# Kernel tuning notes

Hardware: AMD Instinct MI355X
Metric: run time of the kernel (lower is better)

The kernel has to match this reference:

```python
import jax, jax.numpy as jnp
import numpy as np
from jax import lax

N_LAYERS = 30
KERNEL = 5
MU = 255.0  # quantization_channels=256 -> mu = 255
DILATIONS = [(2 ** k) % 10 for k in range(N_LAYERS)]  # 2^k mod (n_layers/n_cycles)


def causal_conv1d(x, w, b, dilation):
    # x: [B,1,T], w: [1,1,K], b: [1]; left-pad so output is causal, same length.
    pad = (w.shape[-1] - 1) * dilation
    xp = jnp.pad(x, ((0, 0), (0, 0), (pad, 0)))
    y = lax.conv_general_dilated(xp, w, window_strides=(1,), padding='VALID',
                                 rhs_dilation=(dilation,),
                                 dimension_numbers=('NCH', 'OIH', 'NCH'))
    return y + b[None, :, None]


def setup_inputs() -> dict:
    key = jax.random.key(0)
    ks = jax.random.split(key, 12)
    B, T = 8, 262144
    s = 0.2  # keep gated activations away from saturation
    return {
        'x': jax.random.normal(ks[0], (B, 1, T), dtype=jnp.float32),
        'causal_w': jax.random.normal(ks[1], (1, 1, KERNEL), jnp.float32) * s,
        'causal_b': jnp.zeros((1,), jnp.float32),
        'filter_w': jax.random.normal(ks[2], (N_LAYERS, 1, 1, KERNEL), jnp.float32) * s,
        'filter_b': jax.random.normal(ks[3], (N_LAYERS, 1), jnp.float32) * s,
        'gate_w': jax.random.normal(ks[4], (N_LAYERS, 1, 1, KERNEL), jnp.float32) * s,
        'gate_b': jax.random.normal(ks[5], (N_LAYERS, 1), jnp.float32) * s,
        'res_w': jax.random.normal(ks[6], (N_LAYERS, 1, 1, 1), jnp.float32) * s,
        'res_b': jax.random.normal(ks[7], (N_LAYERS, 1), jnp.float32) * s,
        'conv1_w': jax.random.normal(ks[8], (1, 1, 1), jnp.float32) * s,
        'conv1_b': jnp.zeros((1,), jnp.float32),
        'conv2_w': jax.random.normal(ks[9], (1, 1, 1), jnp.float32) * s,
        'conv2_b': jnp.zeros((1,), jnp.float32),
    }


def reference(x, causal_w, causal_b, filter_w, filter_b, gate_w, gate_b,
              res_w, res_b, conv1_w, conv1_b, conv2_w, conv2_b):
    h = causal_conv1d(x, causal_w, causal_b, 1)
    skip_sum = jnp.zeros_like(h)
    for k in range(N_LAYERS):  # fixed small layer loop; dilation is static per layer
        d = DILATIONS[k]
        f = jnp.tanh(causal_conv1d(h, filter_w[k], filter_b[k], d))
        g = jax.nn.sigmoid(causal_conv1d(h, gate_w[k], gate_b[k], d))
        z = f * g
        skip_sum = skip_sum + z
        # 1x1 residual conv (1 channel) = scale + bias, then residual add
        h = z * res_w[k][0, 0, 0] + res_b[k][0] + h
    out = jax.nn.relu(skip_sum) * conv1_w[0, 0, 0] + conv1_b[0]
    out = jax.nn.relu(out) * conv2_w[0, 0, 0] + conv2_b[0]
    # mu-law expanding
    out = jnp.sign(out) * (jnp.power(1.0 + MU, jnp.abs(out)) - 1.0) / MU
    return jax.nn.softmax(out, axis=-1)
```

## Files before the change

### kernel.cpp

```cpp
#include <hip/hip_runtime.h>
#include <cmath>

#define T_LEN 262144
#define NROW 8
#define NL 30
#define NT 512
#define PPT 3
#define EXT (NT * PPT * 2)
#define HALO 576
#define TILE (EXT - HALO)
#define PB ((T_LEN + TILE - 1) / TILE)
#define PAD 32
#define CH 4096
#define RB (T_LEN / CH)
#define NB2 (NROW * RB)

#define EIGHT_LN2 5.545177444479562f

__device__ __forceinline__ float fast_rcp(float x) { return __builtin_amdgcn_rcpf(x); }

__device__ __forceinline__ void gated_pair(float afx, float afy, float agx, float agy,
                                           float& zx, float& zy)
{
    const float e1x = __expf(afx + afx);
    const float e1y = __expf(afy + afy);
    const float e2x = __expf(-agx);
    const float e2y = __expf(-agy);
    const float Dx = (e1x + 1.0f) * (1.0f + e2x);
    const float Dy = (e1y + 1.0f) * (1.0f + e2y);
    const float r  = fast_rcp(Dx * Dy);
    zx = (e1x - 1.0f) * Dy * r;
    zy = (e1y - 1.0f) * Dx * r;
}

template<int D>
__device__ __forceinline__ void layer_pair(
    int k,
    const float* __restrict__ fw, const float* __restrict__ fb,
    const float* __restrict__ gw, const float* __restrict__ gb,
    const float* __restrict__ rw, const float* __restrict__ rb,
    const float* __restrict__ src, float* __restrict__ dst,
    float2 (&h)[PPT], float2 (&skip)[PPT], int tid, bool writeback)
{
    const float f0 = fw[k*5+0], f1 = fw[k*5+1], f2 = fw[k*5+2], f3 = fw[k*5+3], f4 = fw[k*5+4];
    const float fbk = fb[k];
    const float g0 = gw[k*5+0], g1 = gw[k*5+1], g2 = gw[k*5+2], g3 = gw[k*5+3], g4 = gw[k*5+4];
    const float gbk = gb[k];
    const float rwk = rw[k], rbk = rb[k];

    #pragma unroll
    for (int p = 0; p < PPT; ++p) {
        const int i2 = 2 * (tid + p * NT);
        const float2 v0 = *(const float2*)&src[i2 - 4*D];
        const float2 v1 = *(const float2*)&src[i2 - 3*D];
        const float2 v2 = *(const float2*)&src[i2 - 2*D];
        const float2 v3 = *(const float2*)&src[i2 -   D];
        const float2 v4 = h[p];

        float afx = fbk, afy = fbk;
        afx = fmaf(f0, v0.x, afx); afy = fmaf(f0, v0.y, afy);
        afx = fmaf(f1, v1.x, afx); afy = fmaf(f1, v1.y, afy);
        afx = fmaf(f2, v2.x, afx); afy = fmaf(f2, v2.y, afy);
        afx = fmaf(f3, v3.x, afx); afy = fmaf(f3, v3.y, afy);
        afx = fmaf(f4, v4.x, afx); afy = fmaf(f4, v4.y, afy);
        float agx = gbk, agy = gbk;
        agx = fmaf(g0, v0.x, agx); agy = fmaf(g0, v0.y, agy);
        agx = fmaf(g1, v1.x, agx); agy = fmaf(g1, v1.y, agy);
        agx = fmaf(g2, v2.x, agx); agy = fmaf(g2, v2.y, agy);
        agx = fmaf(g3, v3.x, agx); agy = fmaf(g3, v3.y, agy);
        agx = fmaf(g4, v4.x, agx); agy = fmaf(g4, v4.y, agy);

        float zx, zy;
        gated_pair(afx, afy, agx, agy, zx, zy);
        skip[p].x += zx; skip[p].y += zy;
        h[p].x = fmaf(zx, rwk, rbk) + v4.x;
        h[p].y = fmaf(zy, rwk, rbk) + v4.y;
    }
    if (writeback) {
        #pragma unroll
        for (int p = 0; p < PPT; ++p)
            *(float2*)&dst[2 * (tid + p * NT)] = h[p];
        __syncthreads();
    }
}

__device__ __forceinline__ void layer_pair_d1(
    int k,
    const float* __restrict__ fw, const float* __restrict__ fb,
    const float* __restrict__ gw, const float* __restrict__ gb,
    const float* __restrict__ rw, const float* __restrict__ rb,
    const float* __restrict__ src, float* __restrict__ dst,
    float2 (&h)[PPT], float2 (&skip)[PPT], int tid)
{
    const float f0 = fw[k*5+0], f1 = fw[k*5+1], f2 = fw[k*5+2], f3 = fw[k*5+3], f4 = fw[k*5+4];
    const float fbk = fb[k];
    const float g0 = gw[k*5+0], g1 = gw[k*5+1], g2 = gw[k*5+2], g3 = gw[k*5+3], g4 = gw[k*5+4];
    const float gbk = gb[k];
    const float rwk = rw[k], rbk = rb[k];

    #pragma unroll
    for (int p = 0; p < PPT; ++p) {
        const int i2 = 2 * (tid + p * NT);
        const float2 a = *(const float2*)&src[i2 - 4];
        const float2 b = *(const float2*)&src[i2 - 2];
        const float2 c = h[p];

        float afx = fbk, afy = fbk, agx = gbk, agy = gbk;
        afx = fmaf(f0, a.x, afx); afy = fmaf(f0, a.y, afy);
        afx = fmaf(f1, a.y, afx); afy = fmaf(f1, b.x, afy);
        afx = fmaf(f2, b.x, afx); afy = fmaf(f2, b.y, afy);
        afx = fmaf(f3, b.y, afx); afy = fmaf(f3, c.x, afy);
        afx = fmaf(f4, c.x, afx); afy = fmaf(f4, c.y, afy);
        agx = fmaf(g0, a.x, agx); agy = fmaf(g0, a.y, agy);
        agx = fmaf(g1, a.y, agx); agy = fmaf(g1, b.x, agy);
        agx = fmaf(g2, b.x, agx); agy = fmaf(g2, b.y, agy);
        agx = fmaf(g3, b.y, agx); agy = fmaf(g3, c.x, agy);
        agx = fmaf(g4, c.x, agx); agy = fmaf(g4, c.y, agy);

        float zx, zy;
        gated_pair(afx, afy, agx, agy, zx, zy);
        skip[p].x += zx; skip[p].y += zy;
        h[p].x = fmaf(zx, rwk, rbk) + c.x;
        h[p].y = fmaf(zy, rwk, rbk) + c.y;
    }
    #pragma unroll
    for (int p = 0; p < PPT; ++p)
        *(float2*)&dst[2 * (tid + p * NT)] = h[p];
    __syncthreads();
}

__global__ __launch_bounds__(NT, 8)
void k_wavenet(const float* __restrict__ x,
               const float* __restrict__ cw,  const float* __restrict__ cb,
               const float* __restrict__ fw,  const float* __restrict__ fb,
               const float* __restrict__ gw,  const float* __restrict__ gb,
               const float* __restrict__ rw,  const float* __restrict__ rb,
               const float* __restrict__ c1w, const float* __restrict__ c1b,
               const float* __restrict__ c2w, const float* __restrict__ c2b,
               float* __restrict__ eout, float* __restrict__ partsum)
{
    __shared__ float hrawA[PAD + EXT];
    __shared__ float hrawB[PAD + EXT];
    __shared__ float reds[NT / 64];
    float* bufA = hrawA + PAD;
    float* bufB = hrawB + PAD;

    const int tid  = threadIdx.x;
    const int row  = blockIdx.x / PB;
    const int tile = blockIdx.x % PB;
    const int t0   = tile * TILE;

    if (tid < PAD) { hrawA[tid] = 0.0f; hrawB[tid] = 0.0f; }

    const float* xr = x + (size_t)row * T_LEN;
    float2 h[PPT], skip[PPT];
    #pragma unroll
    for (int p = 0; p < PPT; ++p) {
        const int i2 = 2 * (tid + p * NT);
        const int g = t0 - HALO + i2;
        float2 v;
        v.x = (g     >= 0 && g     < T_LEN) ? xr[g]     : 0.0f;
        v.y = (g + 1 >= 0 && g + 1 < T_LEN) ? xr[g + 1] : 0.0f;
        *(float2*)&bufA[i2] = v;
        h[p] = v;
        skip[p].x = 0.0f; skip[p].y = 0.0f;
    }
    __syncthreads();

    {
        const float w0 = cw[0], w1 = cw[1], w2 = cw[2], w3 = cw[3], w4 = cw[4];
        const float b  = cb[0];
        #pragma unroll
        for (int p = 0; p < PPT; ++p) {
            const int i2 = 2 * (tid + p * NT);
            const float2 a = *(const float2*)&bufA[i2 - 4];
            const float2 bb = *(const float2*)&bufA[i2 - 2];
            const float2 c = h[p];
            float ax = b, ay = b;
            ax = fmaf(w0, a.x, ax);  ay = fmaf(w0, a.y, ay);
            ax = fmaf(w1, a.y, ax);  ay = fmaf(w1, bb.x, ay);
            ax = fmaf(w2, bb.x, ax); ay = fmaf(w2, bb.y, ay);
            ax = fmaf(w3, bb.y, ax); ay = fmaf(w3, c.x, ay);
            ax = fmaf(w4, c.x, ax);  ay = fmaf(w4, c.y, ay);
            h[p].x = ax; h[p].y = ay;
        }
        #pragma unroll
        for (int p = 0; p < PPT; ++p)
            *(float2*)&bufB[2 * (tid + p * NT)] = h[p];
        __syncthreads();
    }

    layer_pair_d1(0, fw, fb, gw, gb, rw, rb, bufB, bufA, h, skip, tid);
    int k = 1;
    #pragma unroll 1
    for (int c = 0; c < 7; ++c) {
        layer_pair<2>(k+0, fw, fb, gw, gb, rw, rb, bufA, bufB, h, skip, tid, true);
        layer_pair<4>(k+1, fw, fb, gw, gb, rw, rb, bufB, bufA, h, skip, tid, true);
        layer_pair<8>(k+2, fw, fb, gw, gb, rw, rb, bufA, bufB, h, skip, tid, true);
        layer_pair<6>(k+3, fw, fb, gw, gb, rw, rb, bufB, bufA, h, skip, tid, true);
        k += 4;
    }
    layer_pair<2>(29, fw, fb, gw, gb, rw, rb, bufA, bufB, h, skip, tid, false);

    const float w1 = c1w[0], b1 = c1b[0], w2 = c2w[0], b2 = c2b[0];
    float s = 0.0f;
    float* er = eout + (size_t)row * T_LEN;
    #pragma unroll
    for (int p = 0; p < PPT; ++p) {
        const int i2 = 2 * (tid + p * NT);
        if (i2 >= HALO) {
            const int t = t0 + i2 - HALO;
            if (t < T_LEN) {
                float ox = fmaf(fmaxf(skip[p].x, 0.0f), w1, b1);
                float oy = fmaf(fmaxf(skip[p].y, 0.0f), w1, b1);
                ox = fmaf(fmaxf(ox, 0.0f), w2, b2);
                oy = fmaf(fmaxf(oy, 0.0f), w2, b2);
                float vx = (__expf(EIGHT_LN2 * fabsf(ox)) - 1.0f) * (1.0f / 255.0f);
                float vy = (__expf(EIGHT_LN2 * fabsf(oy)) - 1.0f) * (1.0f / 255.0f);
                vx = copysignf(vx, ox);
                vy = copysignf(vy, oy);
                const float ex = __expf(vx);
                const float ey = __expf(vy);
                float2 e; e.x = ex; e.y = ey;
                *(float2*)&er[t] = e;
                s += ex + ey;
            }
        }
    }
    #pragma unroll
    for (int off = 32; off >= 1; off >>= 1)
        s += __shfl_xor(s, off, 64);
    if ((tid & 63) == 0) reds[tid >> 6] = s;
    __syncthreads();
    if (tid == 0) {
        float ss = 0.0f;
        #pragma unroll
        for (int w = 0; w < NT / 64; ++w) ss += reds[w];
        partsum[blockIdx.x] = ss;
    }
}

__global__ __launch_bounds__(256)
void k_scale(float* __restrict__ ebuf, const float* __restrict__ partsum)
{
    const int tid = threadIdx.x;
    const int row = blockIdx.x / RB;

    __shared__ float red[4];
    float s = 0.0f;
    for (int j = tid; j < PB; j += 256) s += partsum[row * PB + j];
    #pragma unroll
    for (int off = 32; off >= 1; off >>= 1)
        s += __shfl_xor(s, off, 64);
    if ((tid & 63) == 0) red[tid >> 6] = s;
    __syncthreads();
    const float tot = (red[0] + red[1]) + (red[2] + red[3]);
    const float inv = 1.0f / tot;

    float4* vp = (float4*)(ebuf + (size_t)blockIdx.x * CH);
    #pragma unroll
    for (int q = 0; q < 4; ++q) {
        float4 v = vp[tid + q * 256];
        v.x *= inv; v.y *= inv; v.z *= inv; v.w *= inv;
        vp[tid + q * 256] = v;
    }
}

extern "C" void kernel_launch(void* const* d_in, const int* in_sizes, int n_in,
                              void* d_out, int out_size, void* d_ws, size_t ws_size,
                              hipStream_t stream)
{
    const float* x   = (const float*)d_in[0];
    const float* cw  = (const float*)d_in[1];
    const float* cb  = (const float*)d_in[2];
    const float* fw  = (const float*)d_in[3];
    const float* fb  = (const float*)d_in[4];
    const float* gw  = (const float*)d_in[5];
    const float* gb  = (const float*)d_in[6];
    const float* rw  = (const float*)d_in[7];
    const float* rb  = (const float*)d_in[8];
    const float* c1w = (const float*)d_in[9];
    const float* c1b = (const float*)d_in[10];
    const float* c2w = (const float*)d_in[11];
    const float* c2b = (const float*)d_in[12];

    float* eout    = (float*)d_out;
    float* partsum = (float*)d_ws;

    k_wavenet<<<NROW * PB, NT, 0, stream>>>(x, cw, cb, fw, fb, gw, gb, rw, rb,
                                            c1w, c1b, c2w, c2b, eout, partsum);
    k_scale<<<NB2, 256, 0, stream>>>(eout, partsum);
}
```

Baseline: 153.8 us.

## Enlarge per-thread tile, skip halo cone work, and use exp2 gating math

Raises points per thread from 3 to 4, so each block's extended tile grows and the fixed halo is a smaller share of it. Adds a per-layer cutoff table so that threads whose first pair lies in the shrinking halo region skip computing it. Replaces the paired tanh·sigmoid evaluation with a per-element exp2-based form that shares one reciprocal, and moves the stores inside the compute loop. This risks more register pressure and a larger shared-memory footprint per block, which could reduce occupancy, and the halo skip leaves stale values in the buffers that must never be read.

```diff
diff --git a/kernel.cpp b/kernel.cpp
--- a/kernel.cpp
+++ b/kernel.cpp
@@ -5,7 +5,7 @@
 #define NROW 8
 #define NL 30
 #define NT 512
-#define PPT 3
+#define PPT 4
 #define EXT (NT * PPT * 2)
 #define HALO 576
 #define TILE (EXT - HALO)
@@ -15,27 +15,32 @@
 #define RB (T_LEN / CH)
 #define NB2 (NROW * RB)
 
-#define EIGHT_LN2 5.545177444479562f
+#define NEG2LOG2E -2.885390082f
+#define NEGLOG2E  -1.4426950409f
+
+#if __has_builtin(__builtin_amdgcn_exp2f)
+#define EXP2(x) __builtin_amdgcn_exp2f(x)
+#else
+#define EXP2(x) __expf(0.6931471805599453f * (x))
+#endif
 
 __device__ __forceinline__ float fast_rcp(float x) { return __builtin_amdgcn_rcpf(x); }
 
-__device__ __forceinline__ void gated_pair(float afx, float afy, float agx, float agy,
-                                           float& zx, float& zy)
-{
-    const float e1x = __expf(afx + afx);
-    const float e1y = __expf(afy + afy);
-    const float e2x = __expf(-agx);
-    const float e2y = __expf(-agy);
-    const float Dx = (e1x + 1.0f) * (1.0f + e2x);
-    const float Dy = (e1y + 1.0f) * (1.0f + e2y);
-    const float r  = fast_rcp(Dx * Dy);
-    zx = (e1x - 1.0f) * Dy * r;
-    zy = (e1y - 1.0f) * Dx * r;
+__device__ const int c_cut[NL] = {
+      8,  16,  32,  64,  88,  96, 112, 144, 168, 176,
+    192, 224, 248, 256, 272, 304, 328, 336, 352, 384,
+    408, 416, 432, 464, 488, 496, 512, 544, 568, 576};
+
+__device__ __forceinline__ float gated(float af, float ag)
+{
+    const float u = EXP2(af * NEG2LOG2E);
+    const float w = EXP2(ag * NEGLOG2E);
+    return (1.0f - u) * fast_rcp((1.0f + u) * (1.0f + w));
 }
 
 template<int D>
 __device__ __forceinline__ void layer_pair(
-    int k,
+    int k, int cut,
     const float* __restrict__ fw, const float* __restrict__ fb,
     const float* __restrict__ gw, const float* __restrict__ gb,
     const float* __restrict__ rw, const float* __restrict__ rb,
@@ -51,6 +56,8 @@
     #pragma unroll
     for (int p = 0; p < PPT; ++p) {
         const int i2 = 2 * (tid + p * NT);
+        if (p == 0 && (i2 + 1) < cut) continue;
+
         const float2 v0 = *(const float2*)&src[i2 - 4*D];
         const float2 v1 = *(const float2*)&src[i2 - 3*D];
         const float2 v2 = *(const float2*)&src[i2 - 2*D];
@@ -70,18 +77,14 @@
         agx = fmaf(g3, v3.x, agx); agy = fmaf(g3, v3.y, agy);
         agx = fmaf(g4, v4.x, agx); agy = fmaf(g4, v4.y, agy);
 
-        float zx, zy;
-        gated_pair(afx, afy, agx, agy, zx, zy);
+        const float zx = gated(afx, agx);
+        const float zy = gated(afy, agy);
         skip[p].x += zx; skip[p].y += zy;
         h[p].x = fmaf(zx, rwk, rbk) + v4.x;
         h[p].y = fmaf(zy, rwk, rbk) + v4.y;
-    }
-    if (writeback) {
-        #pragma unroll
-        for (int p = 0; p < PPT; ++p)
-            *(float2*)&dst[2 * (tid + p * NT)] = h[p];
-        __syncthreads();
-    }
+        if (writeback) *(float2*)&dst[i2] = h[p];
+    }
+    if (writeback) __syncthreads();
 }
 
 __device__ __forceinline__ void layer_pair_d1(
@@ -117,15 +120,13 @@
         agx = fmaf(g3, b.y, agx); agy = fmaf(g3, c.x, agy);
         agx = fmaf(g4, c.x, agx); agy = fmaf(g4, c.y, agy);
 
-        float zx, zy;
-        gated_pair(afx, afy, agx, agy, zx, zy);
+        const float zx = gated(afx, agx);
+        const float zy = gated(afy, agy);
         skip[p].x += zx; skip[p].y += zy;
         h[p].x = fmaf(zx, rwk, rbk) + c.x;
         h[p].y = fmaf(zy, rwk, rbk) + c.y;
-    }
-    #pragma unroll
-    for (int p = 0; p < PPT; ++p)
-        *(float2*)&dst[2 * (tid + p * NT)] = h[p];
+        *(float2*)&dst[i2] = h[p];
+    }
     __syncthreads();
 }
 
@@ -194,13 +195,13 @@
     int k = 1;
     #pragma unroll 1
     for (int c = 0; c < 7; ++c) {
-        layer_pair<2>(k+0, fw, fb, gw, gb, rw, rb, bufA, bufB, h, skip, tid, true);
-        layer_pair<4>(k+1, fw, fb, gw, gb, rw, rb, bufB, bufA, h, skip, tid, true);
-        layer_pair<8>(k+2, fw, fb, gw, gb, rw, rb, bufA, bufB, h, skip, tid, true);
-        layer_pair<6>(k+3, fw, fb, gw, gb, rw, rb, bufB, bufA, h, skip, tid, true);
+        layer_pair<2>(k+0, c_cut[k+0], fw, fb, gw, gb, rw, rb, bufA, bufB, h, skip, tid, true);
+        layer_pair<4>(k+1, c_cut[k+1], fw, fb, gw, gb, rw, rb, bufB, bufA, h, skip, tid, true);
+        layer_pair<8>(k+2, c_cut[k+2], fw, fb, gw, gb, rw, rb, bufA, bufB, h, skip, tid, true);
+        layer_pair<6>(k+3, c_cut[k+3], fw, fb, gw, gb, rw, rb, bufB, bufA, h, skip, tid, true);
         k += 4;
     }
-    layer_pair<2>(29, fw, fb, gw, gb, rw, rb, bufA, bufB, h, skip, tid, false);
+    layer_pair<2>(29, c_cut[29], fw, fb, gw, gb, rw, rb, bufA, bufB, h, skip, tid, false);
 
     const float w1 = c1w[0], b1 = c1b[0], w2 = c2w[0], b2 = c2b[0];
     float s = 0.0f;
@@ -215,8 +216,8 @@
                 float oy = fmaf(fmaxf(skip[p].y, 0.0f), w1, b1);
                 ox = fmaf(fmaxf(ox, 0.0f), w2, b2);
                 oy = fmaf(fmaxf(oy, 0.0f), w2, b2);
-                float vx = (__expf(EIGHT_LN2 * fabsf(ox)) - 1.0f) * (1.0f / 255.0f);
-                float vy = (__expf(EIGHT_LN2 * fabsf(oy)) - 1.0f) * (1.0f / 255.0f);
+                float vx = fmaf(EXP2(8.0f * fabsf(ox)), (1.0f/255.0f), -(1.0f/255.0f));
+                float vy = fmaf(EXP2(8.0f * fabsf(oy)), (1.0f/255.0f), -(1.0f/255.0f));
                 vx = copysignf(vx, ox);
                 vy = copysignf(vy, oy);
                 const float ex = __expf(vx);
@@ -228,8 +229,7 @@
         }
     }
     #pragma unroll
-    for (int off = 32; off >= 1; off >>= 1)
-        s += __shfl_xor(s, off, 64);
+    for (int off = 32; off >= 1; off >>= 1) s += __shfl_xor(s, off, 64);
     if ((tid & 63) == 0) reds[tid >> 6] = s;
     __syncthreads();
     if (tid == 0) {
@@ -250,8 +250,7 @@
     float s = 0.0f;
     for (int j = tid; j < PB; j += 256) s += partsum[row * PB + j];
     #pragma unroll
-    for (int off = 32; off >= 1; off >>= 1)
-        s += __shfl_xor(s, off, 64);
+    for (int off = 32; off >= 1; off >>= 1) s += __shfl_xor(s, off, 64);
     if ((tid & 63) == 0) red[tid >> 6] = s;
     __syncthreads();
     const float tot = (red[0] + red[1]) + (red[2] + red[3]);
```

After: 155.1 us. No clear change (+0.9%).
